# Kernel optimization log

Hardware: AMD Instinct MI355X
Metric: run time of the kernel (lower is better)

Reference implementation:

```python
import jax, jax.numpy as jnp
import numpy as np

POOLED = 7      # kernel_size
SCALE = 0.25    # spatial_scale
GMAX = 2        # upper bound of adaptive sampling grid (box sizes chosen so ceil(roi/7) <= 2)


def setup_inputs() -> dict:
    key = jax.random.key(0)
    k1, k2, k3, k4, k5, k6 = jax.random.split(key, 6)
    B, C, H, W, K = 4, 256, 128, 128, 1000
    features = jax.random.normal(k1, (B, C, H, W), dtype=jnp.float32)
    img = H / SCALE  # 512.0: image-space extent
    bidx = jax.random.randint(k2, (K,), 0, B).astype(jnp.float32)
    bw = jax.random.uniform(k3, (K,), minval=8.0, maxval=56.0)
    bh = jax.random.uniform(k4, (K,), minval=8.0, maxval=56.0)
    x1 = jax.random.uniform(k5, (K,), minval=0.0, maxval=img - 56.0)
    y1 = jax.random.uniform(k6, (K,), minval=0.0, maxval=img - 56.0)
    boxes = jnp.stack([bidx, x1, y1, x1 + bw, y1 + bh], axis=1)
    return {"features": features, "boxes": boxes}


def _sample_coords(start, bin_sz, grid):
    # start/bin_sz/grid: [K] -> coords [K, POOLED, GMAX]
    p = jnp.arange(POOLED, dtype=jnp.float32)
    i = jnp.arange(GMAX, dtype=jnp.float32)
    return (start[:, None, None] + p[None, :, None] * bin_sz[:, None, None]
            + (i[None, None, :] + 0.5) * bin_sz[:, None, None] / grid[:, None, None])


def roi_align(features, boxes):
    B, C, H, W = features.shape
    K = boxes.shape[0]
    b = boxes[:, 0].astype(jnp.int32)
    x1, y1, x2, y2 = (boxes[:, i] * SCALE for i in (1, 2, 3, 4))
    # aligned=False: no -0.5 offset, clamp roi size to >= 1
    roi_w = jnp.maximum(x2 - x1, 1.0)
    roi_h = jnp.maximum(y2 - y1, 1.0)
    bin_w = roi_w / POOLED
    bin_h = roi_h / POOLED
    # sampling_ratio = -1 -> adaptive grid = ceil(roi_size / pooled)
    gh = jnp.ceil(roi_h / POOLED)
    gw = jnp.ceil(roi_w / POOLED)

    y = _sample_coords(y1, bin_h, gh)  # [K,7,GMAX]
    x = _sample_coords(x1, bin_w, gw)  # [K,7,GMAX]
    vy = (jnp.arange(GMAX)[None, None, :] < gh[:, None, None])  # [K,1,GMAX]
    vx = (jnp.arange(GMAX)[None, None, :] < gw[:, None, None])

    # full sample grid [K, 7, GMAX, 7, GMAX] -> flatten to [K, P]
    shp = (K, POOLED, GMAX, POOLED, GMAX)
    Y = jnp.broadcast_to(y[:, :, :, None, None], shp).reshape(K, -1)
    X = jnp.broadcast_to(x[:, None, None, :, :], shp).reshape(K, -1)
    V = jnp.broadcast_to(vy[:, :, :, None, None] & vx[:, None, None, :, :], shp).reshape(K, -1)

    # bilinear interpolation, torchvision boundary semantics
    inval = (Y < -1.0) | (Y > H) | (X < -1.0) | (X > W)
    Yc = jnp.clip(Y, 0.0)
    Xc = jnp.clip(X, 0.0)
    yl = jnp.minimum(Yc.astype(jnp.int32), H - 1)
    xl = jnp.minimum(Xc.astype(jnp.int32), W - 1)
    yh = jnp.minimum(yl + 1, H - 1)
    xh = jnp.minimum(xl + 1, W - 1)
    Yc = jnp.where(yl >= H - 1, yl.astype(jnp.float32), Yc)
    Xc = jnp.where(xl >= W - 1, xl.astype(jnp.float32), Xc)
    ly = Yc - yl
    lx = Xc - xl
    hy = 1.0 - ly
    hx = 1.0 - lx
    m = jnp.where(inval | (~V), 0.0, 1.0)
    w1 = hy * hx * m; w2 = hy * lx * m; w3 = ly * hx * m; w4 = ly * lx * m

    def gather(yi, xi):
        # advanced indexing: [K,P] indices -> [K,P,C]
        return features[b[:, None], :, yi, xi]

    val = (w1[..., None] * gather(yl, xl) + w2[..., None] * gather(yl, xh)
           + w3[..., None] * gather(yh, xl) + w4[..., None] * gather(yh, xh))  # [K,P,C]
    val = val.reshape(K, POOLED, GMAX, POOLED, GMAX, C)
    out = val.sum(axis=(2, 4)) / (gh * gw)[:, None, None, None]  # [K,7,7,C]
    return jnp.transpose(out, (0, 3, 1, 2))  # [K,C,7,7]


def reference(features, boxes):
    return roi_align(features, boxes)
```

## Files before the change

### kernel.cpp

```cpp
#include <hip/hip_runtime.h>

#define POOLED 7
#define SCALE  0.25f
#define CCH    256
#define HH     128
#define WW     128
#define HW     (HH * WW)

#define NCH    16
#define NBLK_PER_BOX (CCH / NCH)
#define PATCH_H 15
#define PATCH_W 16
#define ROWSTRIDE 17
#define CHSTRIDE (PATCH_H * ROWSTRIDE)

__global__ __launch_bounds__(256) void roi_align_kernel(
    const float* __restrict__ feat,
    const float* __restrict__ boxes,
    float* __restrict__ out,
    int K)
{
    __shared__ float patch[NCH * CHSTRIDE];

    int bx    = blockIdx.x;
    int k     = bx >> 4;
    int chunk = bx & 15;
    if (k >= K) return;
    int t = threadIdx.x;

    const float* box = boxes + (size_t)k * 5;
    int   b  = (int)box[0];
    float x1 = box[1] * SCALE;
    float y1 = box[2] * SCALE;
    float x2 = box[3] * SCALE;
    float y2 = box[4] * SCALE;

    float roi_w = fmaxf(x2 - x1, 1.0f);
    float roi_h = fmaxf(y2 - y1, 1.0f);
    float bin_w = roi_w * (1.0f / POOLED);
    float bin_h = roi_h * (1.0f / POOLED);
    int gw = (int)ceilf(roi_w * (1.0f / POOLED));
    int gh = (int)ceilf(roi_h * (1.0f / POOLED));
    float inv_gh = 1.0f / (float)gh;
    float inv_gw = 1.0f / (float)gw;
    int ns = gh * gw;

    float ymin = y1 + (0.5f) * bin_h * inv_gh;
    float ymax = y1 + 6 * bin_h + ((gh - 1) + 0.5f) * bin_h * inv_gh;
    float xmin = x1 + (0.5f) * bin_w * inv_gw;

    int ylo = min((int)fmaxf(ymin, 0.0f), HH - 1);
    int xlo = min((int)fmaxf(xmin, 0.0f), WW - 1);
    int ylmax = min((int)fmaxf(ymax, 0.0f), HH - 1);
    int h_p = min(ylmax + 1, HH - 1) - ylo + 1;
    if (h_p > PATCH_H) h_p = PATCH_H;

    int p  = t & 63;
    int pc = min(p, 48);
    int pw = pc % POOLED;
    int ph = pc / POOLED;
    int c4 = t >> 6;

    float wa[4], wb[4], wc_[4], wd[4];
    int   oa[4], ob[4], oc[4], od[4];

#pragma unroll
    for (int s = 0; s < 4; ++s) {
        int iy = s % gh;
        int ix = s / gh;

        float y = y1 + ph * bin_h + (iy + 0.5f) * bin_h * inv_gh;
        float x = x1 + pw * bin_w + (ix + 0.5f) * bin_w * inv_gw;
        bool valid = (y >= -1.0f) && (y <= (float)HH) && (x >= -1.0f) && (x <= (float)WW);

        float yc = fmaxf(y, 0.0f);
        int yl = min((int)yc, HH - 1);
        int yh2 = min(yl + 1, HH - 1);
        float ly = (yl >= HH - 1) ? 0.0f : (yc - (float)yl);
        float hy = 1.0f - ly;

        float xc = fmaxf(x, 0.0f);
        int xl = min((int)xc, WW - 1);
        int xh2 = min(xl + 1, WW - 1);
        float lx = (xl >= WW - 1) ? 0.0f : (xc - (float)xl);
        float hx = 1.0f - lx;

        float m = valid ? 1.0f : 0.0f;
        wa[s]  = hy * hx * m;
        wb[s]  = hy * lx * m;
        wc_[s] = ly * hx * m;
        wd[s]  = ly * lx * m;

        int ry  = max(0, min(yl  - ylo, PATCH_H - 1));
        int ryh = max(0, min(yh2 - ylo, PATCH_H - 1));
        int rxl = max(0, min(xl  - xlo, PATCH_W - 1));
        int rxh = max(0, min(xh2 - xlo, PATCH_W - 1));
        oa[s] = ry  * ROWSTRIDE + rxl;
        ob[s] = ry  * ROWSTRIDE + rxh;
        oc[s] = ryh * ROWSTRIDE + rxl;
        od[s] = ryh * ROWSTRIDE + rxh;
    }

    int lch  = t >> 4;
    int lcol = t & 15;
    int xcol = min(xlo + lcol, WW - 1);
    int chbase = chunk * NCH;

    {
        int chg = chbase + lch;
        const float* g = feat + ((size_t)b * CCH + chg) * HW + xcol;
        float* lp = patch + lch * CHSTRIDE + lcol;
        for (int r = 0; r < h_p; ++r) {
            int yr = min(ylo + r, HH - 1);
            lp[r * ROWSTRIDE] = g[yr * WW];
        }
    }
    __syncthreads();

    if (p < 49) {
        const float* cp = patch + (c4 * 4) * CHSTRIDE;
        float acc0 = 0.0f, acc1 = 0.0f, acc2 = 0.0f, acc3 = 0.0f;
#pragma unroll
        for (int s = 0; s < 4; ++s) {
            if (s >= ns) break;
            float w1 = wa[s], w2 = wb[s], w3 = wc_[s], w4 = wd[s];
            int o1 = oa[s], o2 = ob[s], o3 = oc[s], o4 = od[s];
            const float* q0 = cp;
            const float* q1 = cp + CHSTRIDE;
            const float* q2 = cp + 2 * CHSTRIDE;
            const float* q3 = cp + 3 * CHSTRIDE;
            acc0 += w1 * q0[o1] + w2 * q0[o2] + w3 * q0[o3] + w4 * q0[o4];
            acc1 += w1 * q1[o1] + w2 * q1[o2] + w3 * q1[o3] + w4 * q1[o4];
            acc2 += w1 * q2[o1] + w2 * q2[o2] + w3 * q2[o3] + w4 * q2[o4];
            acc3 += w1 * q3[o1] + w2 * q3[o2] + w3 * q3[o3] + w4 * q3[o4];
        }
        float sc = inv_gh * inv_gw;
        float* obase = out + ((size_t)k * CCH + chbase + c4 * 4) * 49 + p;
        obase[0]      = acc0 * sc;
        obase[49]     = acc1 * sc;
        obase[2 * 49] = acc2 * sc;
        obase[3 * 49] = acc3 * sc;
    }
}

extern "C" void kernel_launch(void* const* d_in, const int* in_sizes, int n_in,
                              void* d_out, int out_size, void* d_ws, size_t ws_size,
                              hipStream_t stream) {
    const float* feat  = (const float*)d_in[0];
    const float* boxes = (const float*)d_in[1];
    float* out = (float*)d_out;

    int K = in_sizes[1] / 5;
    int blocks = K * NBLK_PER_BOX;
    roi_align_kernel<<<blocks, 256, 0, stream>>>(feat, boxes, out, K);
}
```

Baseline: 136.6 us.

## Use channel-innermost shared patch with float4 reads and two chunks per block

Shared memory is switched from a channel-major to a pixel-major layout with the channel index innermost (padded to 20), so each thread reads its four channels with one float4 LDS per bilinear tap. Each block now handles 32 channels in two sequential 16-channel chunks, which halves the block count and reuses the per-box weight computation. The weight loop now exits early past the real sample count, and row clamps use h_p. The cost is an extra barrier per chunk and strided 4-byte shared stores that may cause bank conflicts during the fill.

```diff
diff --git a/kernel.cpp b/kernel.cpp
--- a/kernel.cpp
+++ b/kernel.cpp
@@ -7,12 +7,14 @@
 #define WW     128
 #define HW     (HH * WW)
 
-#define NCH    16
-#define NBLK_PER_BOX (CCH / NCH)
-#define PATCH_H 15
-#define PATCH_W 16
-#define ROWSTRIDE 17
-#define CHSTRIDE (PATCH_H * ROWSTRIDE)
+#define NCH      16
+#define NCHUNK   2
+#define NBLK_PER_BOX (CCH / (NCH * NCHUNK))
+#define PATCH_H  15
+#define PATCH_W  16
+#define PIXROW   17
+#define NPIX     (14 * PIXROW + 16)
+#define CHPAD    20
 
 __global__ __launch_bounds__(256) void roi_align_kernel(
     const float* __restrict__ feat,
@@ -20,11 +22,11 @@
     float* __restrict__ out,
     int K)
 {
-    __shared__ float patch[NCH * CHSTRIDE];
+    __shared__ float patch[NPIX * CHPAD];
 
-    int bx    = blockIdx.x;
-    int k     = bx >> 4;
-    int chunk = bx & 15;
+    int bx = blockIdx.x;
+    int k  = bx >> 3;
+    int cb = (bx & 7) * (NCH * NCHUNK);
     if (k >= K) return;
     int t = threadIdx.x;
 
@@ -45,9 +47,9 @@
     float inv_gw = 1.0f / (float)gw;
     int ns = gh * gw;
 
-    float ymin = y1 + (0.5f) * bin_h * inv_gh;
+    float ymin = y1 + 0.5f * bin_h * inv_gh;
     float ymax = y1 + 6 * bin_h + ((gh - 1) + 0.5f) * bin_h * inv_gh;
-    float xmin = x1 + (0.5f) * bin_w * inv_gw;
+    float xmin = x1 + 0.5f * bin_w * inv_gw;
 
     int ylo = min((int)fmaxf(ymin, 0.0f), HH - 1);
     int xlo = min((int)fmaxf(xmin, 0.0f), WW - 1);
@@ -66,6 +68,7 @@
 
 #pragma unroll
     for (int s = 0; s < 4; ++s) {
+        if (s >= ns) break;
         int iy = s % gh;
         int ix = s / gh;
 
@@ -91,55 +94,55 @@
         wc_[s] = ly * hx * m;
         wd[s]  = ly * lx * m;
 
-        int ry  = max(0, min(yl  - ylo, PATCH_H - 1));
-        int ryh = max(0, min(yh2 - ylo, PATCH_H - 1));
+        int ry  = max(0, min(yl  - ylo, h_p - 1));
+        int ryh = max(0, min(yh2 - ylo, h_p - 1));
         int rxl = max(0, min(xl  - xlo, PATCH_W - 1));
         int rxh = max(0, min(xh2 - xlo, PATCH_W - 1));
-        oa[s] = ry  * ROWSTRIDE + rxl;
-        ob[s] = ry  * ROWSTRIDE + rxh;
-        oc[s] = ryh * ROWSTRIDE + rxl;
-        od[s] = ryh * ROWSTRIDE + rxh;
+        oa[s] = (ry  * PIXROW + rxl) * CHPAD;
+        ob[s] = (ry  * PIXROW + rxh) * CHPAD;
+        oc[s] = (ryh * PIXROW + rxl) * CHPAD;
+        od[s] = (ryh * PIXROW + rxh) * CHPAD;
     }
 
     int lch  = t >> 4;
     int lcol = t & 15;
     int xcol = min(xlo + lcol, WW - 1);
-    int chbase = chunk * NCH;
+    float sc = inv_gh * inv_gw;
 
-    {
-        int chg = chbase + lch;
-        const float* g = feat + ((size_t)b * CCH + chg) * HW + xcol;
-        float* lp = patch + lch * CHSTRIDE + lcol;
-        for (int r = 0; r < h_p; ++r) {
-            int yr = min(ylo + r, HH - 1);
-            lp[r * ROWSTRIDE] = g[yr * WW];
+    for (int ch = 0; ch < NCHUNK; ++ch) {
+        if (ch) __syncthreads();
+
+        {
+            const float* g = feat + ((size_t)b * CCH + cb + ch * NCH + lch) * HW + xcol;
+            float* lp = patch + lcol * CHPAD + lch;
+            for (int r = 0; r < h_p; ++r) {
+                lp[r * (PIXROW * CHPAD)] = g[(ylo + r) * WW];
+            }
         }
-    }
-    __syncthreads();
+        __syncthreads();
 
-    if (p < 49) {
-        const float* cp = patch + (c4 * 4) * CHSTRIDE;
-        float acc0 = 0.0f, acc1 = 0.0f, acc2 = 0.0f, acc3 = 0.0f;
+        if (p < 49) {
+            float4 acc = {0.0f, 0.0f, 0.0f, 0.0f};
+            const float* cp = patch + c4 * 4;
 #pragma unroll
-        for (int s = 0; s < 4; ++s) {
-            if (s >= ns) break;
-            float w1 = wa[s], w2 = wb[s], w3 = wc_[s], w4 = wd[s];
-            int o1 = oa[s], o2 = ob[s], o3 = oc[s], o4 = od[s];
-            const float* q0 = cp;
-            const float* q1 = cp + CHSTRIDE;
-            const float* q2 = cp + 2 * CHSTRIDE;
-            const float* q3 = cp + 3 * CHSTRIDE;
-            acc0 += w1 * q0[o1] + w2 * q0[o2] + w3 * q0[o3] + w4 * q0[o4];
-            acc1 += w1 * q1[o1] + w2 * q1[o2] + w3 * q1[o3] + w4 * q1[o4];
-            acc2 += w1 * q2[o1] + w2 * q2[o2] + w3 * q2[o3] + w4 * q2[o4];
-            acc3 += w1 * q3[o1] + w2 * q3[o2] + w3 * q3[o3] + w4 * q3[o4];
+            for (int s = 0; s < 4; ++s) {
+                if (s >= ns) break;
+                float4 va = *(const float4*)(cp + oa[s]);
+                float4 vb = *(const float4*)(cp + ob[s]);
+                float4 vc = *(const float4*)(cp + oc[s]);
+                float4 vd = *(const float4*)(cp + od[s]);
+                float w1 = wa[s], w2 = wb[s], w3 = wc_[s], w4 = wd[s];
+                acc.x += w1 * va.x + w2 * vb.x + w3 * vc.x + w4 * vd.x;
+                acc.y += w1 * va.y + w2 * vb.y + w3 * vc.y + w4 * vd.y;
+                acc.z += w1 * va.z + w2 * vb.z + w3 * vc.z + w4 * vd.z;
+                acc.w += w1 * va.w + w2 * vb.w + w3 * vc.w + w4 * vd.w;
+            }
+            float* obase = out + ((size_t)k * CCH + cb + ch * NCH + c4 * 4) * 49 + p;
+            obase[0]      = acc.x * sc;
+            obase[49]     = acc.y * sc;
+            obase[2 * 49] = acc.z * sc;
+            obase[3 * 49] = acc.w * sc;
         }
-        float sc = inv_gh * inv_gw;
-        float* obase = out + ((size_t)k * CCH + chbase + c4 * 4) * 49 + p;
-        obase[0]      = acc0 * sc;
-        obase[49]     = acc1 * sc;
-        obase[2 * 49] = acc2 * sc;
-        obase[3 * 49] = acc3 * sc;
     }
 }
 
```

New measurement: 133.4 us. -2.4%, faster.
